# Kernel tuning notes

Hardware: AMD Instinct MI355X
Metric: run time of the kernel (lower is better)

Reference implementation:

```python
import jax, jax.numpy as jnp
import numpy as np

N = 20000   # nodes
E = 320000  # edges
G = 64      # graphs in batch
IN = 256    # in_dim
H = 256     # hidden_dim1
C = 2       # n_classes


def setup_inputs() -> dict:
    key = jax.random.key(0)
    ks = jax.random.split(key, 12)
    h = jax.random.normal(ks[0], (N, IN), jnp.float32)
    src = jax.random.randint(ks[1], (E,), 0, N)
    dst = jax.random.randint(ks[2], (E,), 0, N)
    graph_id = jnp.sort(jax.random.randint(ks[3], (N,), 0, G))
    s_in = 1.0 / np.sqrt(IN)
    s_h = 1.0 / np.sqrt(H)
    W_conv = jax.random.normal(ks[4], (IN, H), jnp.float32) * s_in
    b_conv = jnp.zeros((H,), jnp.float32)
    w_gate = jax.random.normal(ks[5], (H, 1), jnp.float32) * s_h
    b_gate = jnp.zeros((1,), jnp.float32)
    W1 = jax.random.normal(ks[6], (H, H), jnp.float32) * s_h
    b1 = jnp.zeros((H,), jnp.float32)
    W2 = jax.random.normal(ks[7], (H, C), jnp.float32) * s_h
    b2 = jnp.zeros((C,), jnp.float32)
    return dict(h=h, src=src, dst=dst, graph_id=graph_id, W_conv=W_conv,
                b_conv=b_conv, w_gate=w_gate, b_gate=b_gate, W1=W1, b1=b1,
                W2=W2, b2=b2)


def reference(h, src, dst, graph_id, W_conv, b_conv, w_gate, b_gate, W1, b1, W2, b2):
    ones_e = jnp.ones((E,), jnp.float32)
    # DGL GraphConv, norm='both': D_out^-1/2 on source, D_in^-1/2 on dest
    deg_out = jax.ops.segment_sum(ones_e, src, num_segments=N)
    deg_in = jax.ops.segment_sum(ones_e, dst, num_segments=N)
    hn = h * jax.lax.rsqrt(jnp.maximum(deg_out, 1.0))[:, None]
    hn = hn @ W_conv                       # [N, H] (weight applied before aggregation)
    agg = jax.ops.segment_sum(hn[src], dst, num_segments=N)  # gather + scatter-add
    agg = agg * jax.lax.rsqrt(jnp.maximum(deg_in, 1.0))[:, None] + b_conv
    hr = jax.nn.relu(agg)                  # F.relu after conv1
    # GlobalAttentionPooling: per-graph segment softmax over gate scores
    gate = hr @ w_gate + b_gate            # [N, 1]
    gmax = jax.ops.segment_max(gate, graph_id, num_segments=G)
    e = jnp.exp(gate - gmax[graph_id])
    denom = jax.ops.segment_sum(e, graph_id, num_segments=G)
    att = e / denom[graph_id]              # [N, 1] attention weights (g2)
    hg = jax.ops.segment_sum(att * hr, graph_id, num_segments=G)  # [G, H]
    # classifier heads (dropout is identity at inference)
    a2 = hg @ W1 + b1
    a3 = a2 @ W2 + b2
    return jax.nn.sigmoid(a3), att, hg
```

## Files before the change

### kernel.cpp

```cpp
#include <hip/hip_runtime.h>
#include <hip/hip_bf16.h>
#include <hip/hip_fp16.h>
#include <math.h>

#define NN 20000
#define EE 320000
#define GG 64
#define IND 256
#define HD 256
#define CC 2

typedef __hip_bfloat16 bf16;
typedef __attribute__((ext_vector_type(8))) short short8;
typedef __attribute__((ext_vector_type(4))) float f32x4;

__device__ __forceinline__ float b2f(bf16 x){ return __bfloat162float(x); }
__device__ __forceinline__ float bits2f(unsigned short b){
    union{ float f; unsigned u; } v; v.u = ((unsigned)b) << 16; return v.f;
}
__device__ __forceinline__ short f2bs(float x){
    union{ bf16 b; short s; } u; u.b = __float2bfloat16(x); return u.s;
}
__device__ __forceinline__ float ldf3(const void* p, size_t i, int c){
    if (c == 1) return b2f(((const bf16*)p)[i]);
    if (c == 2) return __half2float(((const __half*)p)[i]);
    return ((const float*)p)[i];
}
__device__ __forceinline__ int idec(const void* p, int i, int c){
    if (c == 1) return (int)(((const long long*)p)[i]);
    if (c == 2) return (int)(((const float*)p)[i]);
    if (c == 3) return (int)__half2float(((const __half*)p)[i]);
    return ((const int*)p)[i];
}

__global__ __launch_bounds__(256) void k_detect(const void* src, const void* dst,
                         const void* gid,
                         const unsigned short* h, const unsigned short* Wc,
                         const unsigned short* wg, const unsigned short* W1,
                         const unsigned short* W2, const unsigned short* bc,
                         int* icode, int* dcode, int* zero_base){
    int blk = blockIdx.x;
    if (blk >= 4){
        int idx = (blk-4)*256 + threadIdx.x;
        const int total = 3*NN + GG*HD;
        for (int i = idx; i < total; i += 60*256) zero_base[i] = 0;
        return;
    }
    if (blk < 3){
        if (threadIdx.x != 0) return;
        const void* buf = (blk == 0) ? src : (blk == 1) ? dst : gid;
        int n     = (blk == 2) ? NN : EE;
        int bound = (blk == 2) ? GG : NN;
        int ok64 = 1, ok32 = 1, okf32 = 1, okf16 = 1;
        const long long* p64 = (const long long*)buf;
        for (int i = 0; i < 64; i++){
            long long v = p64[n/8 + i];
            if (v < 0 || v >= (long long)bound) ok64 = 0;
        }
        const int* p32 = (const int*)buf;
        const unsigned* pu = (const unsigned*)buf;
        for (int i = 0; i < 64; i++){
            int v = p32[n/4 + i];
            if (v < 0 || v >= bound) ok32 = 0;
            float f = __uint_as_float(pu[n/4 + i]);
            if (!(f >= 0.f && f < (float)bound)) okf32 = 0;
        }
        const __half* ph = (const __half*)buf;
        for (int i = 0; i < 64; i++){
            float f = __half2float(ph[n/2 + i]);
            if (!(f >= 0.f && f < (float)bound)) okf16 = 0;
        }
        icode[blk] = ok64 ? 1 : (ok32 ? 0 : (okf32 ? 2 : (okf16 ? 3 : 0)));
    } else {
        int t = threadIdx.x; if (t >= 6) return;
        const unsigned short* p = t==0?h:t==1?Wc:t==2?wg:t==3?W1:t==4?W2:bc;
        int cb = 0, cf = 0, nz = 0;
        for (int i = 0; i < 128; i += 2){
            unsigned u = p[i];
            nz += (u != 0);
            int e8 = (u >> 7) & 0xFF;
            int e5 = (u >> 10) & 0x1F;
            cb += (e8 >= 100 && e8 <= 141);
            cf += (e5 >= 4 && e5 <= 22);
        }
        dcode[t] = (nz < 8) ? 0 : (cb >= 60) ? 1 : ((cf >= 60) ? 2 : 0);
    }
}

__global__ void k_prep(const void* src_r, const void* dst_r, const void* gid_r,
                       const int* __restrict__ icode,
                       int* __restrict__ gid_i,
                       int* cnt_out, int* cnt_in){
    int i = blockIdx.x*256 + threadIdx.x;
    if (i < NN) gid_i[i] = idec(gid_r, i, icode[2]);
    if (i >= EE) return;
    int s = idec(src_r, i, icode[0]);
    int d = idec(dst_r, i, icode[1]);
    if ((unsigned)s < NN) atomicAdd(&cnt_out[s], 1);
    if ((unsigned)d < NN) atomicAdd(&cnt_in[d], 1);
}

__global__ __launch_bounds__(1024) void k_scan(const int* __restrict__ cnt_out,
                                               const int* __restrict__ cnt_in,
                                               const int* __restrict__ gid,
                                               float* rs_out, float* rs_in,
                                               int* __restrict__ row_start,
                                               int* gstart, int* gend){
    int t = threadIdx.x;
    for (int i = t; i < NN; i += 1024){
        rs_out[i] = rsqrtf(fmaxf((float)cnt_out[i], 1.f));
        rs_in[i]  = rsqrtf(fmaxf((float)cnt_in[i], 1.f));
    }
    __shared__ int part[1024];
    const int per = (NN + 1023)/1024;
    int lo = t*per, hi = min(lo+per, NN);
    int s = 0;
    for (int i = lo; i < hi; i++) s += cnt_in[i];
    part[t] = s; __syncthreads();
    for (int off = 1; off < 1024; off <<= 1){
        int v = (t >= off) ? part[t-off] : 0;
        __syncthreads();
        part[t] += v;
        __syncthreads();
    }
    int base = part[t] - s;
    for (int i = lo; i < hi; i++){ row_start[i] = base; base += cnt_in[i]; }
    if (t == 1023) row_start[NN] = part[1023];
    __shared__ int ls[GG+1];
    if (t <= GG){
        int a = 0, b = NN;
        while (a < b){
            int mid = (a + b) >> 1;
            if (gid[mid] < t) a = mid + 1; else b = mid;
        }
        ls[t] = a;
    }
    __syncthreads();
    if (t < GG){ gstart[t] = ls[t]; gend[t] = ls[t+1]; }
}

__global__ void k_fill(const void* src_r, const void* dst_r,
                       const int* __restrict__ icode,
                       const int* __restrict__ row_start, int* __restrict__ cursor,
                       int* __restrict__ csr_src){
    int e = blockIdx.x*256 + threadIdx.x;
    if (e >= EE) return;
    int s = idec(src_r, e, icode[0]);
    int d = idec(dst_r, e, icode[1]);
    if ((unsigned)s >= NN || (unsigned)d >= NN) return;
    int pos = atomicAdd(&cursor[d], 1);
    csr_src[row_start[d] + pos] = s;
}

__global__ void k_wprep(const void* __restrict__ W, const int* __restrict__ dcode,
                        bf16* __restrict__ Wb){
    int k = blockIdx.x;
    int n = threadIdx.x;
    Wb[(size_t)n*IND + k] = __float2bfloat16(ldf3(W, (size_t)k*HD + n, dcode[1]));
}

__global__ __launch_bounds__(256) void k_gemm1m(const void* __restrict__ h,
                                                const bf16* __restrict__ Wb,
                                                const float* __restrict__ rs_out,
                                                const int* __restrict__ dcode,
                                                bf16* __restrict__ hn){
    int fh = dcode[0];
    int tid = threadIdx.x;
    int wave = tid >> 6, lane = tid & 63;
    int q = lane >> 4, mr = lane & 15;
    int row0 = blockIdx.x * 32;
    int ncol0 = wave * 64;
    f32x4 acc[2][4] = {};
    const float* hf = (const float*)h;
    #pragma unroll
    for (int k0 = 0; k0 < IND; k0 += 32){
        short8 a[2], b[4];
        if (fh == 0){
            #pragma unroll
            for (int mi = 0; mi < 2; mi++){
                int r = row0 + mi*16 + mr;
                const float4* p = (const float4*)(hf + (size_t)r*IND + k0 + q*8);
                float4 v0 = p[0], v1 = p[1];
                a[mi][0] = f2bs(v0.x); a[mi][1] = f2bs(v0.y);
                a[mi][2] = f2bs(v0.z); a[mi][3] = f2bs(v0.w);
                a[mi][4] = f2bs(v1.x); a[mi][5] = f2bs(v1.y);
                a[mi][6] = f2bs(v1.z); a[mi][7] = f2bs(v1.w);
            }
        } else {
            #pragma unroll
            for (int mi = 0; mi < 2; mi++){
                int r = row0 + mi*16 + mr;
                #pragma unroll
                for (int j = 0; j < 8; j++)
                    a[mi][j] = f2bs(ldf3(h, (size_t)r*IND + k0 + q*8 + j, fh));
            }
        }
        #pragma unroll
        for (int ni = 0; ni < 4; ni++)
            b[ni] = *reinterpret_cast<const short8*>(
                        Wb + (size_t)(ncol0 + ni*16 + mr)*IND + k0 + q*8);
        #pragma unroll
        for (int mi = 0; mi < 2; mi++)
            #pragma unroll
            for (int ni = 0; ni < 4; ni++)
                acc[mi][ni] = __builtin_amdgcn_mfma_f32_16x16x32_bf16(
                                  a[mi], b[ni], acc[mi][ni], 0, 0, 0);
    }
    #pragma unroll
    for (int mi = 0; mi < 2; mi++){
        int rowb = row0 + mi*16 + q*4;
        #pragma unroll
        for (int r = 0; r < 4; r++){
            int row = rowb + r;
            float rs = rs_out[row];
            #pragma unroll
            for (int ni = 0; ni < 4; ni++)
                hn[(size_t)row*HD + ncol0 + ni*16 + mr] =
                    __float2bfloat16(acc[mi][ni][r] * rs);
        }
    }
}

__global__ __launch_bounds__(256) void k_gather(const bf16* __restrict__ hn,
                                                const float* __restrict__ rs_in,
                                                const int* __restrict__ row_start,
                                                const int* __restrict__ csr_src,
                                                const void* __restrict__ b_conv,
                                                const void* __restrict__ w_gate,
                                                const void* __restrict__ b_gate,
                                                const int* __restrict__ dcode,
                                                float* __restrict__ hr,
                                                float* __restrict__ gate){
    int wave = threadIdx.x >> 6, lane = threadIdx.x & 63;
    int n = blockIdx.x*4 + wave;
    if (n >= NN) return;
    int lo = row_start[n], hi = row_start[n+1];
    float ax = 0.f, ay = 0.f, az = 0.f, aw = 0.f;
    int j = lo;
    for (; j + 8 <= hi; j += 8){
        int s0 = csr_src[j+0], s1 = csr_src[j+1], s2 = csr_src[j+2], s3 = csr_src[j+3];
        int s4 = csr_src[j+4], s5 = csr_src[j+5], s6 = csr_src[j+6], s7 = csr_src[j+7];
        ushort4 u0 = ((const ushort4*)(hn + (size_t)s0*HD))[lane];
        ushort4 u1 = ((const ushort4*)(hn + (size_t)s1*HD))[lane];
        ushort4 u2 = ((const ushort4*)(hn + (size_t)s2*HD))[lane];
        ushort4 u3 = ((const ushort4*)(hn + (size_t)s3*HD))[lane];
        ushort4 u4 = ((const ushort4*)(hn + (size_t)s4*HD))[lane];
        ushort4 u5 = ((const ushort4*)(hn + (size_t)s5*HD))[lane];
        ushort4 u6 = ((const ushort4*)(hn + (size_t)s6*HD))[lane];
        ushort4 u7 = ((const ushort4*)(hn + (size_t)s7*HD))[lane];
        ax += bits2f(u0.x)+bits2f(u1.x)+bits2f(u2.x)+bits2f(u3.x)
            + bits2f(u4.x)+bits2f(u5.x)+bits2f(u6.x)+bits2f(u7.x);
        ay += bits2f(u0.y)+bits2f(u1.y)+bits2f(u2.y)+bits2f(u3.y)
            + bits2f(u4.y)+bits2f(u5.y)+bits2f(u6.y)+bits2f(u7.y);
        az += bits2f(u0.z)+bits2f(u1.z)+bits2f(u2.z)+bits2f(u3.z)
            + bits2f(u4.z)+bits2f(u5.z)+bits2f(u6.z)+bits2f(u7.z);
        aw += bits2f(u0.w)+bits2f(u1.w)+bits2f(u2.w)+bits2f(u3.w)
            + bits2f(u4.w)+bits2f(u5.w)+bits2f(u6.w)+bits2f(u7.w);
    }
    for (; j < hi; j++){
        int s = csr_src[j];
        ushort4 u = ((const ushort4*)(hn + (size_t)s*HD))[lane];
        ax += bits2f(u.x); ay += bits2f(u.y); az += bits2f(u.z); aw += bits2f(u.w);
    }
    int db = dcode[5], fg = dcode[2];
    float rsn = rs_in[n];
    int c = lane*4;
    ax = fmaxf(fmaf(ax, rsn, ldf3(b_conv, c+0, db)), 0.f);
    ay = fmaxf(fmaf(ay, rsn, ldf3(b_conv, c+1, db)), 0.f);
    az = fmaxf(fmaf(az, rsn, ldf3(b_conv, c+2, db)), 0.f);
    aw = fmaxf(fmaf(aw, rsn, ldf3(b_conv, c+3, db)), 0.f);
    float4 v; v.x = ax; v.y = ay; v.z = az; v.w = aw;
    ((float4*)(hr + (size_t)n*HD))[lane] = v;
    float g = ax*ldf3(w_gate, c+0, fg) + ay*ldf3(w_gate, c+1, fg)
            + az*ldf3(w_gate, c+2, fg) + aw*ldf3(w_gate, c+3, fg);
    #pragma unroll
    for (int off = 32; off; off >>= 1) g += __shfl_down(g, off);
    if (lane == 0) gate[n] = g + ldf3(b_gate, 0, db);
}

__global__ __launch_bounds__(256) void k_soft(const int* __restrict__ gstart,
                                              const int* __restrict__ gend,
                                              float* __restrict__ gate,
                                              float* __restrict__ out_att){
    int g = blockIdx.x, t = threadIdx.x;
    int lo = gstart[g], hi = gend[g];
    if (lo >= hi) return;
    __shared__ float sm[256];
    float m = -INFINITY;
    for (int n = lo + t; n < hi; n += 256) m = fmaxf(m, gate[n]);
    sm[t] = m; __syncthreads();
    for (int s = 128; s; s >>= 1){ if (t < s) sm[t] = fmaxf(sm[t], sm[t+s]); __syncthreads(); }
    m = sm[0]; __syncthreads();
    float acc = 0.f;
    for (int n = lo + t; n < hi; n += 256){
        float e = expf(gate[n] - m);
        gate[n] = e;
        acc += e;
    }
    sm[t] = acc; __syncthreads();
    for (int s = 128; s; s >>= 1){ if (t < s) sm[t] += sm[t+s]; __syncthreads(); }
    float inv = 1.f / sm[0];
    for (int n = lo + t; n < hi; n += 256){
        float a = gate[n] * inv;
        gate[n] = a;
        out_att[n] = a;
    }
}

__global__ __launch_bounds__(256) void k_hg(const float* __restrict__ att,
                                            const float* __restrict__ hr,
                                            const int* __restrict__ gstart,
                                            const int* __restrict__ gend,
                                            float* __restrict__ hg){
    int g = blockIdx.x >> 3, part = blockIdx.x & 7;
    int c = threadIdx.x;
    int s = gstart[g], en = gend[g];
    int len = en - s;
    if (len <= 0) return;
    int chunk = (len + 7) >> 3;
    int lo = s + part*chunk, hi = min(lo + chunk, en);
    if (lo >= hi) return;
    float acc = 0.f;
    for (int n = lo; n < hi; n++) acc += att[n] * hr[(size_t)n*HD + c];
    atomicAdd(&hg[g*HD + c], acc);
}

__global__ __launch_bounds__(256) void k_cls(const float* __restrict__ hg,
                                             const void* __restrict__ W1,
                                             const void* __restrict__ b1,
                                             const void* __restrict__ W2,
                                             const void* __restrict__ b2,
                                             const int* __restrict__ dcode,
                                             float* __restrict__ out0,
                                             float* __restrict__ out_hg){
    int f1 = dcode[3], f2 = dcode[4], db = dcode[5];
    int g = blockIdx.x, tid = threadIdx.x;
    __shared__ float hs[256];
    float hv = hg[g*HD + tid];
    hs[tid] = hv;
    out_hg[g*HD + tid] = hv;
    __syncthreads();
    float acc = ldf3(b1, tid, db);
    if (f1 == 1){
        const bf16* w = (const bf16*)W1;
        for (int k = 0; k < HD; k++) acc += hs[k]*b2f(w[(size_t)k*HD + tid]);
    } else if (f1 == 2){
        const __half* w = (const __half*)W1;
        for (int k = 0; k < HD; k++) acc += hs[k]*__half2float(w[(size_t)k*HD + tid]);
    } else {
        const float* w = (const float*)W1;
        for (int k = 0; k < HD; k++) acc += hs[k]*w[(size_t)k*HD + tid];
    }
    float p0 = acc * ldf3(W2, tid*CC + 0, f2);
    float p1 = acc * ldf3(W2, tid*CC + 1, f2);
    __shared__ float r0[256], r1[256];
    r0[tid] = p0; r1[tid] = p1; __syncthreads();
    for (int s = 128; s; s >>= 1){
        if (tid < s){ r0[tid] += r0[tid+s]; r1[tid] += r1[tid+s]; }
        __syncthreads();
    }
    if (tid == 0){
        out0[g*CC+0] = 1.f/(1.f + expf(-(r0[0] + ldf3(b2, 0, db))));
        out0[g*CC+1] = 1.f/(1.f + expf(-(r1[0] + ldf3(b2, 1, db))));
    }
}

extern "C" void kernel_launch(void* const* d_in, const int* in_sizes, int n_in,
                              void* d_out, int out_size, void* d_ws, size_t ws_size,
                              hipStream_t stream) {
    const void* h      = d_in[0];
    const void* src_r  = d_in[1];
    const void* dst_r  = d_in[2];
    const void* gid_r  = d_in[3];
    const void* W_conv = d_in[4];
    const void* b_conv = d_in[5];
    const void* w_gate = d_in[6];
    const void* b_gate = d_in[7];
    const void* W1     = d_in[8];
    const void* b1     = d_in[9];
    const void* W2     = d_in[10];
    const void* b2     = d_in[11];

    float* out     = (float*)d_out;
    float* out0    = out;
    float* out_att = out + GG*CC;
    float* out_hg  = out + GG*CC + NN;

    char* w = (char*)d_ws;
    float* hr   = (float*)w;  w += (size_t)NN*HD*sizeof(float);
    bf16*  hn   = (bf16*)w;   w += (size_t)NN*HD*sizeof(bf16);
    bf16*  Wb   = (bf16*)w;   w += (size_t)IND*HD*sizeof(bf16);
    float* rs_o = (float*)w;  w += (size_t)NN*sizeof(float);
    float* rs_i = (float*)w;  w += (size_t)NN*sizeof(float);
    float* gate = (float*)w;  w += (size_t)NN*sizeof(float);
    int* gstart = (int*)w;    w += GG*sizeof(int);
    int* gend   = (int*)w;    w += GG*sizeof(int);
    int* dcode  = (int*)w;    w += 8*sizeof(int);
    int* icode  = (int*)w;    w += 8*sizeof(int);
    int* gid_i  = (int*)w;    w += (size_t)NN*sizeof(int);
    int* cnt_out= (int*)w;    w += (size_t)NN*sizeof(int);
    int* cnt_in = (int*)w;    w += (size_t)NN*sizeof(int);
    int* cursor = (int*)w;    w += (size_t)NN*sizeof(int);
    float* hg   = (float*)w;  w += (size_t)GG*HD*sizeof(float);
    int* rowst  = (int*)w;    w += (size_t)(NN+1)*sizeof(int);
    int* csr    = (int*)w;    w += (size_t)EE*sizeof(int);

    k_detect<<<64, 256, 0, stream>>>(src_r, dst_r, gid_r,
                                     (const unsigned short*)h, (const unsigned short*)W_conv,
                                     (const unsigned short*)w_gate, (const unsigned short*)W1,
                                     (const unsigned short*)W2, (const unsigned short*)b_conv,
                                     icode, dcode, cnt_out);

    k_prep<<<(EE+255)/256, 256, 0, stream>>>(src_r, dst_r, gid_r, icode,
                                             gid_i, cnt_out, cnt_in);
    k_scan<<<1, 1024, 0, stream>>>(cnt_out, cnt_in, gid_i, rs_o, rs_i,
                                   rowst, gstart, gend);
    k_fill<<<(EE+255)/256, 256, 0, stream>>>(src_r, dst_r, icode, rowst, cursor, csr);

    k_wprep<<<IND, HD, 0, stream>>>(W_conv, dcode, Wb);
    k_gemm1m<<<NN/32, 256, 0, stream>>>(h, Wb, rs_o, dcode, hn);

    k_gather<<<(NN+3)/4, 256, 0, stream>>>(hn, rs_i, rowst, csr,
                                           b_conv, w_gate, b_gate, dcode, hr, gate);

    k_soft<<<GG, 256, 0, stream>>>(gstart, gend, gate, out_att);
    k_hg<<<GG*8, 256, 0, stream>>>(gate, hr, gstart, gend, hg);
    k_cls<<<GG, 256, 0, stream>>>(hg, W1, b1, W2, b2, dcode, out0, out_hg);
}
```

Before: 250.0 us.

## Fuse softmax, pooling and classifier into one kernel; merge weight prep into detect

```diff
diff --git a/kernel.cpp b/kernel.cpp
--- a/kernel.cpp
+++ b/kernel.cpp
@@ -32,20 +32,28 @@
     if (c == 3) return (int)__half2float(((const __half*)p)[i]);
     return ((const int*)p)[i];
 }
-
+__device__ __forceinline__ int wdetect(const unsigned short* p){
+    int cb = 0, cf = 0, nz = 0;
+    for (int i = 0; i < 128; i += 2){
+        unsigned u = p[i];
+        nz += (u != 0);
+        int e8 = (u >> 7) & 0xFF;
+        int e5 = (u >> 10) & 0x1F;
+        cb += (e8 >= 100 && e8 <= 141);
+        cf += (e5 >= 4 && e5 <= 22);
+    }
+    return (nz < 8) ? 0 : (cb >= 60) ? 1 : ((cf >= 60) ? 2 : 0);
+}
+
+#define ZBLK 64
 __global__ __launch_bounds__(256) void k_detect(const void* src, const void* dst,
                          const void* gid,
                          const unsigned short* h, const unsigned short* Wc,
                          const unsigned short* wg, const unsigned short* W1,
                          const unsigned short* W2, const unsigned short* bc,
-                         int* icode, int* dcode, int* zero_base){
+                         int* icode, int* dcode, int* zero_base,
+                         bf16* __restrict__ Wb){
     int blk = blockIdx.x;
-    if (blk >= 4){
-        int idx = (blk-4)*256 + threadIdx.x;
-        const int total = 3*NN + GG*HD;
-        for (int i = idx; i < total; i += 60*256) zero_base[i] = 0;
-        return;
-    }
     if (blk < 3){
         if (threadIdx.x != 0) return;
         const void* buf = (blk == 0) ? src : (blk == 1) ? dst : gid;
@@ -71,19 +79,22 @@
             if (!(f >= 0.f && f < (float)bound)) okf16 = 0;
         }
         icode[blk] = ok64 ? 1 : (ok32 ? 0 : (okf32 ? 2 : (okf16 ? 3 : 0)));
-    } else {
+    } else if (blk == 3){
         int t = threadIdx.x; if (t >= 6) return;
         const unsigned short* p = t==0?h:t==1?Wc:t==2?wg:t==3?W1:t==4?W2:bc;
-        int cb = 0, cf = 0, nz = 0;
-        for (int i = 0; i < 128; i += 2){
-            unsigned u = p[i];
-            nz += (u != 0);
-            int e8 = (u >> 7) & 0xFF;
-            int e5 = (u >> 10) & 0x1F;
-            cb += (e8 >= 100 && e8 <= 141);
-            cf += (e5 >= 4 && e5 <= 22);
-        }
-        dcode[t] = (nz < 8) ? 0 : (cb >= 60) ? 1 : ((cf >= 60) ? 2 : 0);
+        dcode[t] = wdetect(p);
+    } else if (blk < 4 + IND){
+        int k = blk - 4;
+        __shared__ int code;
+        if (threadIdx.x == 0) code = wdetect(Wc);
+        __syncthreads();
+        int c = code;
+        int n = threadIdx.x;
+        Wb[(size_t)n*IND + k] = __float2bfloat16(ldf3(Wc, (size_t)k*HD + n, c));
+    } else {
+        int idx = (blk - (4 + IND))*256 + threadIdx.x;
+        const int total = 3*NN;
+        for (int i = idx; i < total; i += ZBLK*256) zero_base[i] = 0;
     }
 }
 
@@ -150,13 +161,6 @@
     if ((unsigned)s >= NN || (unsigned)d >= NN) return;
     int pos = atomicAdd(&cursor[d], 1);
     csr_src[row_start[d] + pos] = s;
-}
-
-__global__ void k_wprep(const void* __restrict__ W, const int* __restrict__ dcode,
-                        bf16* __restrict__ Wb){
-    int k = blockIdx.x;
-    int n = threadIdx.x;
-    Wb[(size_t)n*IND + k] = __float2bfloat16(ldf3(W, (size_t)k*HD + n, dcode[1]));
 }
 
 __global__ __launch_bounds__(256) void k_gemm1m(const void* __restrict__ h,
@@ -278,90 +282,107 @@
     if (lane == 0) gate[n] = g + ldf3(b_gate, 0, db);
 }
 
-__global__ __launch_bounds__(256) void k_soft(const int* __restrict__ gstart,
+__global__ __launch_bounds__(256) void k_pool(const float* __restrict__ gate,
+                                              const float* __restrict__ hr,
+                                              const int* __restrict__ gstart,
                                               const int* __restrict__ gend,
-                                              float* __restrict__ gate,
-                                              float* __restrict__ out_att){
+                                              const void* __restrict__ W1,
+                                              const void* __restrict__ b1,
+                                              const void* __restrict__ W2,
+                                              const void* __restrict__ b2,
+                                              const int* __restrict__ dcode,
+                                              float* __restrict__ out0,
+                                              float* __restrict__ out_att,
+                                              float* __restrict__ out_hg){
     int g = blockIdx.x, t = threadIdx.x;
     int lo = gstart[g], hi = gend[g];
-    if (lo >= hi) return;
+    int len = hi - lo;
     __shared__ float sm[256];
-    float m = -INFINITY;
-    for (int n = lo + t; n < hi; n += 256) m = fmaxf(m, gate[n]);
-    sm[t] = m; __syncthreads();
-    for (int s = 128; s; s >>= 1){ if (t < s) sm[t] = fmaxf(sm[t], sm[t+s]); __syncthreads(); }
-    m = sm[0]; __syncthreads();
-    float acc = 0.f;
-    for (int n = lo + t; n < hi; n += 256){
-        float e = expf(gate[n] - m);
-        gate[n] = e;
-        acc += e;
-    }
-    sm[t] = acc; __syncthreads();
-    for (int s = 128; s; s >>= 1){ if (t < s) sm[t] += sm[t+s]; __syncthreads(); }
-    float inv = 1.f / sm[0];
-    for (int n = lo + t; n < hi; n += 256){
-        float a = gate[n] * inv;
-        gate[n] = a;
-        out_att[n] = a;
-    }
-}
-
-__global__ __launch_bounds__(256) void k_hg(const float* __restrict__ att,
-                                            const float* __restrict__ hr,
-                                            const int* __restrict__ gstart,
-                                            const int* __restrict__ gend,
-                                            float* __restrict__ hg){
-    int g = blockIdx.x >> 3, part = blockIdx.x & 7;
-    int c = threadIdx.x;
-    int s = gstart[g], en = gend[g];
-    int len = en - s;
-    if (len <= 0) return;
-    int chunk = (len + 7) >> 3;
-    int lo = s + part*chunk, hi = min(lo + chunk, en);
-    if (lo >= hi) return;
-    float acc = 0.f;
-    for (int n = lo; n < hi; n++) acc += att[n] * hr[(size_t)n*HD + c];
-    atomicAdd(&hg[g*HD + c], acc);
-}
-
-__global__ __launch_bounds__(256) void k_cls(const float* __restrict__ hg,
-                                             const void* __restrict__ W1,
-                                             const void* __restrict__ b1,
-                                             const void* __restrict__ W2,
-                                             const void* __restrict__ b2,
-                                             const int* __restrict__ dcode,
-                                             float* __restrict__ out0,
-                                             float* __restrict__ out_hg){
+    __shared__ float satt[1024];
+    float hgc = 0.f;
+    if (len > 0){
+        float m = -INFINITY;
+        for (int n = lo + t; n < hi; n += 256) m = fmaxf(m, gate[n]);
+        sm[t] = m; __syncthreads();
+        for (int s = 128; s; s >>= 1){ if (t < s) sm[t] = fmaxf(sm[t], sm[t+s]); __syncthreads(); }
+        m = sm[0]; __syncthreads();
+        float ac = 0.f;
+        for (int n = lo + t; n < hi; n += 256) ac += expf(gate[n] - m);
+        sm[t] = ac; __syncthreads();
+        for (int s = 128; s; s >>= 1){ if (t < s) sm[t] += sm[t+s]; __syncthreads(); }
+        float inv = 1.f / sm[0];
+        for (int n = lo + t; n < hi; n += 256){
+            float a = expf(gate[n] - m) * inv;
+            out_att[n] = a;
+            int idx = n - lo;
+            if (idx < 1024) satt[idx] = a;
+        }
+        __syncthreads();
+        float a0 = 0.f, a1 = 0.f, a2 = 0.f, a3 = 0.f;
+        int i = 0;
+        for (; i + 4 <= len; i += 4){
+            float w0 = (i+0 < 1024) ? satt[i+0] : out_att[lo+i+0];
+            float w1 = (i+1 < 1024) ? satt[i+1] : out_att[lo+i+1];
+            float w2 = (i+2 < 1024) ? satt[i+2] : out_att[lo+i+2];
+            float w3 = (i+3 < 1024) ? satt[i+3] : out_att[lo+i+3];
+            a0 = fmaf(w0, hr[(size_t)(lo+i+0)*HD + t], a0);
+            a1 = fmaf(w1, hr[(size_t)(lo+i+1)*HD + t], a1);
+            a2 = fmaf(w2, hr[(size_t)(lo+i+2)*HD + t], a2);
+            a3 = fmaf(w3, hr[(size_t)(lo+i+3)*HD + t], a3);
+        }
+        for (; i < len; i++){
+            float w0 = (i < 1024) ? satt[i] : out_att[lo+i];
+            a0 = fmaf(w0, hr[(size_t)(lo+i)*HD + t], a0);
+        }
+        hgc = (a0 + a1) + (a2 + a3);
+    }
+    out_hg[g*HD + t] = hgc;
+    __syncthreads();
+    sm[t] = hgc;
+    __syncthreads();
     int f1 = dcode[3], f2 = dcode[4], db = dcode[5];
-    int g = blockIdx.x, tid = threadIdx.x;
-    __shared__ float hs[256];
-    float hv = hg[g*HD + tid];
-    hs[tid] = hv;
-    out_hg[g*HD + tid] = hv;
-    __syncthreads();
-    float acc = ldf3(b1, tid, db);
+    float acc = ldf3(b1, t, db);
     if (f1 == 1){
         const bf16* w = (const bf16*)W1;
-        for (int k = 0; k < HD; k++) acc += hs[k]*b2f(w[(size_t)k*HD + tid]);
+        float c0=0.f,c1=0.f,c2=0.f,c3=0.f;
+        for (int k = 0; k < HD; k += 4){
+            c0 = fmaf(sm[k+0], b2f(w[(size_t)(k+0)*HD + t]), c0);
+            c1 = fmaf(sm[k+1], b2f(w[(size_t)(k+1)*HD + t]), c1);
+            c2 = fmaf(sm[k+2], b2f(w[(size_t)(k+2)*HD + t]), c2);
+            c3 = fmaf(sm[k+3], b2f(w[(size_t)(k+3)*HD + t]), c3);
+        }
+        acc += (c0+c1)+(c2+c3);
     } else if (f1 == 2){
         const __half* w = (const __half*)W1;
-        for (int k = 0; k < HD; k++) acc += hs[k]*__half2float(w[(size_t)k*HD + tid]);
+        float c0=0.f,c1=0.f,c2=0.f,c3=0.f;
+        for (int k = 0; k < HD; k += 4){
+            c0 = fmaf(sm[k+0], __half2float(w[(size_t)(k+0)*HD + t]), c0);
+            c1 = fmaf(sm[k+1], __half2float(w[(size_t)(k+1)*HD + t]), c1);
+            c2 = fmaf(sm[k+2], __half2float(w[(size_t)(k+2)*HD + t]), c2);
+            c3 = fmaf(sm[k+3], __half2float(w[(size_t)(k+3)*HD + t]), c3);
+        }
+        acc += (c0+c1)+(c2+c3);
     } else {
         const float* w = (const float*)W1;
-        for (int k = 0; k < HD; k++) acc += hs[k]*w[(size_t)k*HD + tid];
-    }
-    float p0 = acc * ldf3(W2, tid*CC + 0, f2);
-    float p1 = acc * ldf3(W2, tid*CC + 1, f2);
-    __shared__ float r0[256], r1[256];
-    r0[tid] = p0; r1[tid] = p1; __syncthreads();
+        float c0=0.f,c1=0.f,c2=0.f,c3=0.f;
+        for (int k = 0; k < HD; k += 4){
+            c0 = fmaf(sm[k+0], w[(size_t)(k+0)*HD + t], c0);
+            c1 = fmaf(sm[k+1], w[(size_t)(k+1)*HD + t], c1);
+            c2 = fmaf(sm[k+2], w[(size_t)(k+2)*HD + t], c2);
+            c3 = fmaf(sm[k+3], w[(size_t)(k+3)*HD + t], c3);
+        }
+        acc += (c0+c1)+(c2+c3);
+    }
+    float p0 = acc * ldf3(W2, t*CC + 0, f2);
+    float p1 = acc * ldf3(W2, t*CC + 1, f2);
+    satt[t] = p0; satt[256 + t] = p1; __syncthreads();
     for (int s = 128; s; s >>= 1){
-        if (tid < s){ r0[tid] += r0[tid+s]; r1[tid] += r1[tid+s]; }
+        if (t < s){ satt[t] += satt[t+s]; satt[256+t] += satt[256+t+s]; }
         __syncthreads();
     }
-    if (tid == 0){
-        out0[g*CC+0] = 1.f/(1.f + expf(-(r0[0] + ldf3(b2, 0, db))));
-        out0[g*CC+1] = 1.f/(1.f + expf(-(r1[0] + ldf3(b2, 1, db))));
+    if (t == 0){
+        out0[g*CC+0] = 1.f/(1.f + expf(-(satt[0]   + ldf3(b2, 0, db))));
+        out0[g*CC+1] = 1.f/(1.f + expf(-(satt[256] + ldf3(b2, 1, db))));
     }
 }
 
@@ -401,15 +422,14 @@
     int* cnt_out= (int*)w;    w += (size_t)NN*sizeof(int);
     int* cnt_in = (int*)w;    w += (size_t)NN*sizeof(int);
     int* cursor = (int*)w;    w += (size_t)NN*sizeof(int);
-    float* hg   = (float*)w;  w += (size_t)GG*HD*sizeof(float);
     int* rowst  = (int*)w;    w += (size_t)(NN+1)*sizeof(int);
     int* csr    = (int*)w;    w += (size_t)EE*sizeof(int);
 
-    k_detect<<<64, 256, 0, stream>>>(src_r, dst_r, gid_r,
+    k_detect<<<4 + IND + ZBLK, 256, 0, stream>>>(src_r, dst_r, gid_r,
                                      (const unsigned short*)h, (const unsigned short*)W_conv,
                                      (const unsigned short*)w_gate, (const unsigned short*)W1,
                                      (const unsigned short*)W2, (const unsigned short*)b_conv,
-                                     icode, dcode, cnt_out);
+                                     icode, dcode, cnt_out, Wb);
 
     k_prep<<<(EE+255)/256, 256, 0, stream>>>(src_r, dst_r, gid_r, icode,
                                              gid_i, cnt_out, cnt_in);
@@ -417,13 +437,11 @@
                                    rowst, gstart, gend);
     k_fill<<<(EE+255)/256, 256, 0, stream>>>(src_r, dst_r, icode, rowst, cursor, csr);
 
-    k_wprep<<<IND, HD, 0, stream>>>(W_conv, dcode, Wb);
     k_gemm1m<<<NN/32, 256, 0, stream>>>(h, Wb, rs_o, dcode, hn);
 
     k_gather<<<(NN+3)/4, 256, 0, stream>>>(hn, rs_i, rowst, csr,
                                            b_conv, w_gate, b_gate, dcode, hr, gate);
 
-    k_soft<<<GG, 256, 0, stream>>>(gstart, gend, gate, out_att);
-    k_hg<<<GG*8, 256, 0, stream>>>(gate, hr, gstart, gend, hg);
-    k_cls<<<GG, 256, 0, stream>>>(hg, W1, b1, W2, b2, dcode, out0, out_hg);
-}
+    k_pool<<<GG, 256, 0, stream>>>(gate, hr, gstart, gend,
+                                   W1, b1, W2, b2, dcode, out0, out_att, out_hg);
+}
```

Result: slower. 262.4 us (+5.0%).
